# Kernel tuning notes

Measured on AMD Instinct MI355X. Metric: run time of the kernel, lower is better.

Reference implementation:

```python
import jax, jax.numpy as jnp
import numpy as np
import math

NUM_HEADS = 16
ROPE_BASE = 10000.0

def _rotate_half(t):
    d = t.shape[-1]
    x1, x2 = t[..., : d // 2], t[..., d // 2 :]
    return jnp.concatenate([-x2, x1], axis=-1)

def _rope_tables(seq_len, head_dim, dtype):
    inv_freq = 1.0 / (ROPE_BASE ** (jnp.arange(0, head_dim, 2, dtype=jnp.float32) / head_dim))
    t = jnp.arange(seq_len, dtype=jnp.float32)
    freqs = jnp.einsum('i,j->ij', t, inv_freq)          # [S, d/2]
    emb = jnp.concatenate([freqs, freqs], axis=-1)      # [S, d]
    return jnp.cos(emb).astype(dtype), jnp.sin(emb).astype(dtype)

def setup_inputs() -> dict:
    key = jax.random.key(0)
    ks = jax.random.split(key, 6)
    B, S, HID = 4, 2048, 1024
    x = jax.random.normal(ks[0], (B, S, HID), dtype=jnp.float32)
    w_scale = 0.02
    Wq = jax.random.normal(ks[1], (HID, HID), dtype=jnp.float32) * w_scale
    Wk = jax.random.normal(ks[2], (HID, HID), dtype=jnp.float32) * w_scale
    Wv = jax.random.normal(ks[3], (HID, HID), dtype=jnp.float32) * w_scale
    Wo = jax.random.normal(ks[4], (HID, HID), dtype=jnp.float32) * w_scale
    # ragged valid lengths in [S//2, S] so each sequence is non-trivial
    seq_lens = jax.random.randint(ks[5], (B,), S // 2, S + 1, dtype=jnp.int32)
    return {"x": x, "Wq": Wq, "Wk": Wk, "Wv": Wv, "Wo": Wo, "seq_lens": seq_lens}

def reference(x, Wq, Wk, Wv, Wo, seq_lens):
    B, S, HID = x.shape
    H = NUM_HEADS
    d = HID // H
    scale = 1.0 / math.sqrt(d)

    # qkv projections (nn.Linear, no bias)
    q = (x @ Wq).reshape(B, S, H, d)
    k = (x @ Wk).reshape(B, S, H, d)
    v = (x @ Wv).reshape(B, S, H, d)

    # fused RoPE, positions start at 0 for every sequence (prefill, beg=0)
    cos, sin = _rope_tables(S, d, x.dtype)              # [S, d]
    cos = cos[None, :, None, :]
    sin = sin[None, :, None, :]
    q = q * cos + _rotate_half(q) * sin
    k = k * cos + _rotate_half(k) * sin

    # causal SDPA over ragged batch via padding masks
    scores = jnp.einsum('bqhd,bkhd->bhqk', q, k) * scale  # [B,H,S,S]
    pos = jnp.arange(S)
    causal = pos[:, None] >= pos[None, :]                 # [S,S]
    valid_k = pos[None, :] < seq_lens[:, None]            # [B,S]
    mask = causal[None, None, :, :] & valid_k[:, None, None, :]
    neg = jnp.asarray(-1e9, dtype=scores.dtype)
    attn = jax.nn.softmax(jnp.where(mask, scores, neg), axis=-1)
    out = jnp.einsum('bhqk,bkhd->bqhd', attn, v).reshape(B, S, HID)

    out = out @ Wo
    # zero out padded query positions (they do not exist in CatTensor)
    valid_q = (pos[None, :] < seq_lens[:, None])[..., None]
    return jnp.where(valid_q, out, jnp.zeros((), dtype=out.dtype))
```

## Files before the change

kernel.cpp:

```cpp
#include <hip/hip_runtime.h>
#include <hip/hip_bf16.h>

typedef __attribute__((ext_vector_type(8))) short short8;
typedef __attribute__((ext_vector_type(4))) float f32x4;

constexpr int Bc   = 4;
constexpr int Sc   = 2048;
constexpr int HIDc = 1024;
constexpr int Hc   = 16;
constexpr size_t FB = (size_t)Bc * Sc * HIDc;
constexpr size_t WN = (size_t)HIDc * HIDc;

__device__ __forceinline__ int get_L(const int* seq, int b)
{
    return (seq[1] == 0) ? seq[2 * b] : seq[b];
}

__device__ __forceinline__ short f2bf(float v)
{
    __hip_bfloat16 h = __float2bfloat16(v);
    return *reinterpret_cast<short*>(&h);
}
__device__ __forceinline__ float bf2f(short s)
{
    __hip_bfloat16 h = *reinterpret_cast<__hip_bfloat16*>(&s);
    return __bfloat162float(h);
}
__device__ __forceinline__ unsigned pack2(short a, short b)
{
    return (unsigned)(unsigned short)a | ((unsigned)(unsigned short)b << 16);
}

__global__ __launch_bounds__(256) void split_pass(const float* __restrict__ in,
                                                  short* __restrict__ hi,
                                                  short* __restrict__ lo)
{
    const size_t i8 = ((size_t)blockIdx.x * 256 + threadIdx.x) * 8;
    const float4 u0 = *(const float4*)(in + i8);
    const float4 u1 = *(const float4*)(in + i8 + 4);
    const float v[8] = {u0.x, u0.y, u0.z, u0.w, u1.x, u1.y, u1.z, u1.w};
    short8 h, l;
#pragma unroll
    for (int j = 0; j < 8; j++) {
        const short hb = f2bf(v[j]);
        h[j] = hb;
        l[j] = f2bf(v[j] - bf2f(hb));
    }
    *(short8*)(hi + i8) = h;
    *(short8*)(lo + i8) = l;
}

__global__ __launch_bounds__(256) void rope_split(const float* __restrict__ p,
                                                  short* __restrict__ hi,
                                                  short* __restrict__ lo)
{
    const int idx = blockIdx.x * 256 + threadIdx.x;
    const int jc = idx & 3;
    const int h  = (idx >> 2) & 15;
    const int s  = (idx >> 6) & 2047;
    const int b  = idx >> 17;
    const int j0 = jc * 8;
    const size_t base = ((size_t)(b * Sc + s)) * HIDc + h * 64 + j0;

    const float4 a0 = *(const float4*)(p + base);
    const float4 a1 = *(const float4*)(p + base + 4);
    const float4 b0 = *(const float4*)(p + base + 32);
    const float4 b1 = *(const float4*)(p + base + 36);
    const float x1[8] = {a0.x, a0.y, a0.z, a0.w, a1.x, a1.y, a1.z, a1.w};
    const float x2[8] = {b0.x, b0.y, b0.z, b0.w, b1.x, b1.y, b1.z, b1.w};

    short8 h1, h2, l1, l2;
#pragma unroll
    for (int jj = 0; jj < 8; jj++) {
        const int j = j0 + jj;
        const float ang = (float)s * powf(10000.0f, -(float)j * (1.0f / 32.0f));
        const float cv = cosf(ang);
        const float sv = sinf(ang);
        const float y1 = x1[jj] * cv - x2[jj] * sv;
        const float y2 = x2[jj] * cv + x1[jj] * sv;
        const short hb1 = f2bf(y1), hb2 = f2bf(y2);
        h1[jj] = hb1; l1[jj] = f2bf(y1 - bf2f(hb1));
        h2[jj] = hb2; l2[jj] = f2bf(y2 - bf2f(hb2));
    }
    *(short8*)(hi + base)      = h1;
    *(short8*)(hi + base + 32) = h2;
    *(short8*)(lo + base)      = l1;
    *(short8*)(lo + base + 32) = l2;
}

__global__ __launch_bounds__(256) void vsplit_t(const float* __restrict__ V,
                                                short* __restrict__ th,
                                                short* __restrict__ tl)
{
    __shared__ float T[64][65];
    const int s0 = blockIdx.x * 64;
    const int h  = blockIdx.y & 15;
    const int b  = blockIdx.y >> 4;
    const int t  = threadIdx.x;
    const int r  = t >> 2;
    const int c  = (t & 3) * 16;
#pragma unroll
    for (int j = 0; j < 4; j++) {
        const float4 u = *(const float4*)(V + ((size_t)(b * Sc + s0 + r)) * HIDc + h * 64 + c + j * 4);
        T[r][c + j * 4 + 0] = u.x; T[r][c + j * 4 + 1] = u.y;
        T[r][c + j * 4 + 2] = u.z; T[r][c + j * 4 + 3] = u.w;
    }
    __syncthreads();
    short8 h0, h1, l0, l1;
#pragma unroll
    for (int j = 0; j < 8; j++) {
        const float v = T[c + j][r];
        const short hb = f2bf(v);
        h0[j] = hb; l0[j] = f2bf(v - bf2f(hb));
    }
#pragma unroll
    for (int j = 0; j < 8; j++) {
        const float v = T[c + 8 + j][r];
        const short hb = f2bf(v);
        h1[j] = hb; l1[j] = f2bf(v - bf2f(hb));
    }
    const size_t dst = ((size_t)(b * Hc + h) * 64 + r) * Sc + s0 + c;
    *(short8*)(th + dst)     = h0;
    *(short8*)(th + dst + 8) = h1;
    *(short8*)(tl + dst)     = l0;
    *(short8*)(tl + dst + 8) = l1;
}

__device__ __forceinline__ void wsplit_body(const float* __restrict__ W,
                                            short* __restrict__ th,
                                            short* __restrict__ tl,
                                            float (*T)[65])
{
    const int t  = threadIdx.x;
    const int n0 = blockIdx.x * 64;
    const int k0 = blockIdx.y * 64;
    const int r  = t >> 2;
    const int c  = (t & 3) * 16;
#pragma unroll
    for (int j = 0; j < 4; j++) {
        const float4 u = *(const float4*)(W + (size_t)(k0 + r) * HIDc + n0 + c + j * 4);
        T[r][c + j * 4 + 0] = u.x; T[r][c + j * 4 + 1] = u.y;
        T[r][c + j * 4 + 2] = u.z; T[r][c + j * 4 + 3] = u.w;
    }
    __syncthreads();
    short8 h0, h1, l0, l1;
#pragma unroll
    for (int j = 0; j < 8; j++) {
        const float v = T[c + j][r];
        const short hb = f2bf(v);
        h0[j] = hb; l0[j] = f2bf(v - bf2f(hb));
    }
#pragma unroll
    for (int j = 0; j < 8; j++) {
        const float v = T[c + 8 + j][r];
        const short hb = f2bf(v);
        h1[j] = hb; l1[j] = f2bf(v - bf2f(hb));
    }
    const size_t dst = (size_t)(n0 + r) * HIDc + k0 + c;
    *(short8*)(th + dst)     = h0;
    *(short8*)(th + dst + 8) = h1;
    *(short8*)(tl + dst)     = l0;
    *(short8*)(tl + dst + 8) = l1;
}

__global__ __launch_bounds__(256) void wsplit_t(const float* __restrict__ W,
                                                short* __restrict__ th,
                                                short* __restrict__ tl)
{
    __shared__ float T[64][65];
    wsplit_body(W, th, tl, T);
}

__global__ __launch_bounds__(256) void wsplit4_t(
    const float* __restrict__ W0, const float* __restrict__ W1,
    const float* __restrict__ W2, const float* __restrict__ W3,
    short* __restrict__ out)
{
    __shared__ float T[64][65];
    const int z = blockIdx.z;
    const float* W = (z == 0) ? W0 : (z == 1) ? W1 : (z == 2) ? W2 : W3;
    short* th = out + (size_t)z * 2 * WN;
    wsplit_body(W, th, th + WN, T);
}

__device__ __forceinline__ void gemm_x3_body(
    const short* __restrict__ Ah, const short* __restrict__ Al,
    const short* __restrict__ Bh, const short* __restrict__ Bl,
    float* __restrict__ C, const int* __restrict__ seq,
    const int m0, const int n0,
    short* AhS, short* AlS, short* BhS, short* BlS)
{
    const int t    = threadIdx.x;
    const int lane = t & 63;
    const int wid  = t >> 6;
    const int wr   = (wid >> 1) * 64;
    const int wc   = (wid & 1) * 64;
    const int lr   = lane & 15;
    const int lg   = lane >> 4;

    f32x4 acc[4][4];
#pragma unroll
    for (int mi = 0; mi < 4; mi++)
#pragma unroll
        for (int ni = 0; ni < 4; ni++) acc[mi][ni] = (f32x4)(0.f);

    for (int k0 = 0; k0 < HIDc; k0 += 64) {
        __syncthreads();
#pragma unroll
        for (int i = 0; i < 4; i++) {
            const int o  = i * 4096 + t * 16;
            const int r  = o >> 7;
            const int sc = (o & 127) ^ ((r & 7) << 4);
            const int k  = sc >> 1;
            const size_t ga = (size_t)(m0 + r) * HIDc + k0 + k;
            const size_t gb = (size_t)(n0 + r) * HIDc + k0 + k;
            __builtin_amdgcn_global_load_lds(
                (const __attribute__((address_space(1))) void*)(Ah + ga),
                (__attribute__((address_space(3))) void*)(AhS + (o >> 1)), 16, 0, 0);
            __builtin_amdgcn_global_load_lds(
                (const __attribute__((address_space(1))) void*)(Al + ga),
                (__attribute__((address_space(3))) void*)(AlS + (o >> 1)), 16, 0, 0);
            __builtin_amdgcn_global_load_lds(
                (const __attribute__((address_space(1))) void*)(Bh + gb),
                (__attribute__((address_space(3))) void*)(BhS + (o >> 1)), 16, 0, 0);
            __builtin_amdgcn_global_load_lds(
                (const __attribute__((address_space(1))) void*)(Bl + gb),
                (__attribute__((address_space(3))) void*)(BlS + (o >> 1)), 16, 0, 0);
        }
        __syncthreads();

        short8 a_h[4][2], a_l[4][2];
#pragma unroll
        for (int mi = 0; mi < 4; mi++) {
            const int r = wr + mi * 16 + lr;
#pragma unroll
            for (int kk = 0; kk < 2; kk++) {
                const int cb  = kk * 64 + lg * 16;
                const int off = r * 128 + (cb ^ ((r & 7) << 4));
                a_h[mi][kk] = *(const short8*)((const char*)AhS + off);
                a_l[mi][kk] = *(const short8*)((const char*)AlS + off);
            }
        }
#pragma unroll
        for (int ni = 0; ni < 4; ni++) {
            const int rn = wc + ni * 16 + lr;
            short8 b_h[2], b_l[2];
#pragma unroll
            for (int kk = 0; kk < 2; kk++) {
                const int cb  = kk * 64 + lg * 16;
                const int off = rn * 128 + (cb ^ ((rn & 7) << 4));
                b_h[kk] = *(const short8*)((const char*)BhS + off);
                b_l[kk] = *(const short8*)((const char*)BlS + off);
            }
#pragma unroll
            for (int mi = 0; mi < 4; mi++) {
#pragma unroll
                for (int kk = 0; kk < 2; kk++) {
                    acc[mi][ni] = __builtin_amdgcn_mfma_f32_16x16x32_bf16(
                        a_h[mi][kk], b_h[kk], acc[mi][ni], 0, 0, 0);
                    acc[mi][ni] = __builtin_amdgcn_mfma_f32_16x16x32_bf16(
                        a_h[mi][kk], b_l[kk], acc[mi][ni], 0, 0, 0);
                    acc[mi][ni] = __builtin_amdgcn_mfma_f32_16x16x32_bf16(
                        a_l[mi][kk], b_h[kk], acc[mi][ni], 0, 0, 0);
                }
            }
        }
    }

#pragma unroll
    for (int mi = 0; mi < 4; mi++) {
#pragma unroll
        for (int rr = 0; rr < 4; rr++) {
            const int row = m0 + wr + mi * 16 + lg * 4 + rr;
            bool zero = false;
            if (seq != nullptr) zero = ((row & 2047) >= get_L(seq, row >> 11));
#pragma unroll
            for (int ni = 0; ni < 4; ni++) {
                const float v = zero ? 0.f : acc[mi][ni][rr];
                C[(size_t)row * HIDc + n0 + wc + ni * 16 + lr] = v;
            }
        }
    }
}

__global__ __launch_bounds__(256, 2) void gemm_x3(
    const short* __restrict__ Ah, const short* __restrict__ Al,
    const short* __restrict__ Bh, const short* __restrict__ Bl,
    float* __restrict__ C, const int* __restrict__ seq)
{
    __shared__ alignas(16) short AhS[128 * 64];
    __shared__ alignas(16) short AlS[128 * 64];
    __shared__ alignas(16) short BhS[128 * 64];
    __shared__ alignas(16) short BlS[128 * 64];
    const int F   = blockIdx.x + 8 * blockIdx.y;
    const int xcd = F & 7;
    const int s   = F >> 3;
    const int ly  = xcd + 8 * (s >> 3);
    const int lx  = s & 7;
    gemm_x3_body(Ah, Al, Bh, Bl, C, seq, ly * 128, lx * 128,
                 AhS, AlS, BhS, BlS);
}

__global__ __launch_bounds__(256, 2) void gemm_x3_qkv(
    const short* __restrict__ Ah, const short* __restrict__ Al,
    const short* __restrict__ Wbase, float* __restrict__ Cbase)
{
    __shared__ alignas(16) short AhS[128 * 64];
    __shared__ alignas(16) short AlS[128 * 64];
    __shared__ alignas(16) short BhS[128 * 64];
    __shared__ alignas(16) short BlS[128 * 64];
    const int F   = blockIdx.x + 8 * blockIdx.y + 512 * blockIdx.z;
    const int xcd = F & 7;
    const int s   = F >> 3;
    const int ly  = xcd + 8 * (s / 24);
    const int rem = s % 24;
    const int lx  = rem & 7;
    const int lz  = rem >> 3;
    const short* Bh = Wbase + (size_t)lz * 2 * WN;
    gemm_x3_body(Ah, Al, Bh, Bh + WN, Cbase + (size_t)lz * FB,
                 nullptr, ly * 128, lx * 128, AhS, AlS, BhS, BlS);
}

__global__ __launch_bounds__(256, 3) void attn_mfma_sw(
    const short* __restrict__ Qh, const short* __restrict__ Ql,
    const short* __restrict__ Kh, const short* __restrict__ Kl,
    const short* __restrict__ Vth, const short* __restrict__ Vtl,
    short* __restrict__ Oh, short* __restrict__ Ol,
    const int* __restrict__ seq)
{
    __shared__ alignas(16) short KhS[64 * 64];
    __shared__ alignas(16) short KlS[64 * 64];
    __shared__ alignas(16) short VhS[64 * 64];
    __shared__ alignas(16) short VlS[64 * 64];
    __shared__ alignas(16) short PhS[4][16 * 64];
    __shared__ alignas(16) short PlS[4][16 * 64];

    const int blk  = blockIdx.x;
    const int bh   = blk & 63;
    const int qt   = 31 - (blk >> 6);
    const int h    = bh & 15;
    const int b    = bh >> 4;
    const int q0   = qt * 64;
    const int L    = get_L(seq, b);
    const int t    = threadIdx.x;
    const int w    = t >> 6;
    const int lane = t & 63;
    const int lr   = lane & 15;
    const int lg   = lane >> 4;

    if (q0 >= L) {
        const int r = t >> 2;
        const int c = (t & 3) * 16;
        const size_t base = ((size_t)(b * Sc + q0 + r)) * HIDc + h * 64 + c;
        const short8 z = {0, 0, 0, 0, 0, 0, 0, 0};
        *(short8*)(Oh + base)     = z;
        *(short8*)(Oh + base + 8) = z;
        *(short8*)(Ol + base)     = z;
        *(short8*)(Ol + base + 8) = z;
        return;
    }

    short8 qb_h[2], qb_l[2];
    {
        const size_t qrow = ((size_t)(b * Sc + q0 + w * 16 + lr)) * HIDc + h * 64;
        qb_h[0] = *(const short8*)(Qh + qrow + lg * 8);
        qb_h[1] = *(const short8*)(Qh + qrow + 32 + lg * 8);
        qb_l[0] = *(const short8*)(Ql + qrow + lg * 8);
        qb_l[1] = *(const short8*)(Ql + qrow + 32 + lg * 8);
    }

    f32x4 oacc[4];
#pragma unroll
    for (int t2 = 0; t2 < 4; t2++) oacc[t2] = (f32x4)(0.f);
    float m_s = -1.0e30f, l_s = 0.f;

    const int qpos = q0 + w * 16 + lr;

    const int kend = min(q0 + 64, L);
    for (int kb = 0; kb < kend; kb += 64) {
        __syncthreads();
#pragma unroll
        for (int i = 0; i < 2; i++) {
            const int o  = i * 4096 + t * 16;
            const int r  = o >> 7;
            const int sc = (o & 127) ^ ((r & 7) << 4);
            const int k  = sc >> 1;
            const size_t gk = ((size_t)(b * Sc + kb + r)) * HIDc + h * 64 + k;
            const size_t gv = ((size_t)(b * Hc + h) * 64 + r) * Sc + kb + k;
            __builtin_amdgcn_global_load_lds(
                (const __attribute__((address_space(1))) void*)(Kh + gk),
                (__attribute__((address_space(3))) void*)((char*)KhS + o), 16, 0, 0);
            __builtin_amdgcn_global_load_lds(
                (const __attribute__((address_space(1))) void*)(Kl + gk),
                (__attribute__((address_space(3))) void*)((char*)KlS + o), 16, 0, 0);
            __builtin_amdgcn_global_load_lds(
                (const __attribute__((address_space(1))) void*)(Vth + gv),
                (__attribute__((address_space(3))) void*)((char*)VhS + o), 16, 0, 0);
            __builtin_amdgcn_global_load_lds(
                (const __attribute__((address_space(1))) void*)(Vtl + gv),
                (__attribute__((address_space(3))) void*)((char*)VlS + o), 16, 0, 0);
        }
        __syncthreads();

        f32x4 s4[4];
#pragma unroll
        for (int tt = 0; tt < 4; tt++) s4[tt] = (f32x4)(0.f);
        __builtin_amdgcn_s_setprio(1);
#pragma unroll
        for (int tt = 0; tt < 4; tt++) {
            const int rn = tt * 16 + lr;
#pragma unroll
            for (int kk = 0; kk < 2; kk++) {
                const int off = rn * 128 + ((kk * 64 + lg * 16) ^ ((rn & 7) << 4));
                const short8 ka_h = *(const short8*)((const char*)KhS + off);
                const short8 ka_l = *(const short8*)((const char*)KlS + off);
                s4[tt] = __builtin_amdgcn_mfma_f32_16x16x32_bf16(ka_h, qb_h[kk], s4[tt], 0, 0, 0);
                s4[tt] = __builtin_amdgcn_mfma_f32_16x16x32_bf16(ka_h, qb_l[kk], s4[tt], 0, 0, 0);
                s4[tt] = __builtin_amdgcn_mfma_f32_16x16x32_bf16(ka_l, qb_h[kk], s4[tt], 0, 0, 0);
            }
        }
        __builtin_amdgcn_s_setprio(0);

        float tmax = -1.0e30f;
#pragma unroll
        for (int tt = 0; tt < 4; tt++)
#pragma unroll
            for (int r = 0; r < 4; r++) {
                const int kpos = kb + tt * 16 + lg * 4 + r;
                const bool valid = (kpos <= qpos) && (kpos < L);
                const float v = valid ? s4[tt][r] * 0.125f : -1.0e9f;
                s4[tt][r] = v;
                tmax = fmaxf(tmax, v);
            }
        tmax = fmaxf(tmax, __shfl_xor(tmax, 16));
        tmax = fmaxf(tmax, __shfl_xor(tmax, 32));
        const float mnew  = fmaxf(m_s, tmax);
        const float alpha = __expf(m_s - mnew);
        float psum = 0.f;
#pragma unroll
        for (int tt = 0; tt < 4; tt++)
#pragma unroll
            for (int r = 0; r < 4; r++) {
                const float e = __expf(s4[tt][r] - mnew);
                s4[tt][r] = e;
                psum += e;
            }
        psum += __shfl_xor(psum, 16);
        psum += __shfl_xor(psum, 32);
        l_s = alpha * l_s + psum;
        m_s = mnew;

#pragma unroll
        for (int r = 0; r < 4; r++) {
            const float ar = __shfl(alpha, lg * 4 + r);
#pragma unroll
            for (int t2 = 0; t2 < 4; t2++) oacc[t2][r] *= ar;
        }

#pragma unroll
        for (int tt = 0; tt < 4; tt++) {
            const short h0 = f2bf(s4[tt][0]); const short l0 = f2bf(s4[tt][0] - bf2f(h0));
            const short h1 = f2bf(s4[tt][1]); const short l1 = f2bf(s4[tt][1] - bf2f(h1));
            const short h2 = f2bf(s4[tt][2]); const short l2 = f2bf(s4[tt][2] - bf2f(h2));
            const short h3 = f2bf(s4[tt][3]); const short l3 = f2bf(s4[tt][3] - bf2f(h3));
            const int off = lr * 128 + ((tt * 32 + lg * 8) ^ ((lr & 7) << 4));
            uint2 uh; uh.x = pack2(h0, h1); uh.y = pack2(h2, h3);
            uint2 ul; ul.x = pack2(l0, l1); ul.y = pack2(l2, l3);
            *(uint2*)((char*)&PhS[w][0] + off) = uh;
            *(uint2*)((char*)&PlS[w][0] + off) = ul;
        }

        __builtin_amdgcn_sched_barrier(0);

        short8 pa_h[2], pa_l[2];
#pragma unroll
        for (int kk = 0; kk < 2; kk++) {
            const int poff = lr * 128 + ((kk * 64 + lg * 16) ^ ((lr & 7) << 4));
            pa_h[kk] = *(const short8*)((const char*)&PhS[w][0] + poff);
            pa_l[kk] = *(const short8*)((const char*)&PlS[w][0] + poff);
        }
        __builtin_amdgcn_s_setprio(1);
#pragma unroll
        for (int t2 = 0; t2 < 4; t2++) {
            const int rv = t2 * 16 + lr;
#pragma unroll
            for (int kk = 0; kk < 2; kk++) {
                const int voff = rv * 128 + ((kk * 64 + lg * 16) ^ ((rv & 7) << 4));
                const short8 vb_h = *(const short8*)((const char*)VhS + voff);
                const short8 vb_l = *(const short8*)((const char*)VlS + voff);
                oacc[t2] = __builtin_amdgcn_mfma_f32_16x16x32_bf16(pa_h[kk], vb_h, oacc[t2], 0, 0, 0);
                oacc[t2] = __builtin_amdgcn_mfma_f32_16x16x32_bf16(pa_h[kk], vb_l, oacc[t2], 0, 0, 0);
                oacc[t2] = __builtin_amdgcn_mfma_f32_16x16x32_bf16(pa_l[kk], vb_h, oacc[t2], 0, 0, 0);
            }
        }
        __builtin_amdgcn_s_setprio(0);
    }

#pragma unroll
    for (int r = 0; r < 4; r++) {
        const float lrow = __shfl(l_s, lg * 4 + r);
        const float inv  = 1.0f / lrow;
        const int   row  = q0 + w * 16 + lg * 4 + r;
        const size_t base = ((size_t)(b * Sc + row)) * HIDc + h * 64;
#pragma unroll
        for (int t2 = 0; t2 < 4; t2++) {
            const float v = oacc[t2][r] * inv;
            const short hb = f2bf(v);
            Oh[base + t2 * 16 + lr] = hb;
            Ol[base + t2 * 16 + lr] = f2bf(v - bf2f(hb));
        }
    }
}

__global__ __launch_bounds__(256) void gemm64(
    const float* __restrict__ A, const float* __restrict__ W,
    float* __restrict__ C, const int K, const int N,
    const int* __restrict__ seq)
{
    __shared__ float As[32][68];
    __shared__ float Bs[32][68];

    const int t  = threadIdx.x;
    const int m0 = blockIdx.y * 64;
    const int n0 = blockIdx.x * 64;
    const int ty = t >> 4, tx = t & 15;
    const int ar = t >> 2;
    const int ac = (t & 3) * 8;
    const int wr = t >> 3;
    const int wc = (t & 7) * 8;

    float acc[4][4];
#pragma unroll
    for (int i = 0; i < 4; i++)
#pragma unroll
        for (int j = 0; j < 4; j++) acc[i][j] = 0.f;

    for (int k0 = 0; k0 < K; k0 += 32) {
        __syncthreads();
        {
            const float* p = A + (size_t)(m0 + ar) * K + k0 + ac;
            const float4 u0 = *(const float4*)p;
            const float4 u1 = *(const float4*)(p + 4);
            As[ac + 0][ar] = u0.x; As[ac + 1][ar] = u0.y;
            As[ac + 2][ar] = u0.z; As[ac + 3][ar] = u0.w;
            As[ac + 4][ar] = u1.x; As[ac + 5][ar] = u1.y;
            As[ac + 6][ar] = u1.z; As[ac + 7][ar] = u1.w;
        }
        {
            const float* p = W + (size_t)(k0 + wr) * N + n0 + wc;
            const float4 u0 = *(const float4*)p;
            const float4 u1 = *(const float4*)(p + 4);
            *(float4*)&Bs[wr][wc]     = u0;
            *(float4*)&Bs[wr][wc + 4] = u1;
        }
        __syncthreads();

#pragma unroll 8
        for (int kk = 0; kk < 32; kk++) {
            const float4 a4 = *(const float4*)&As[kk][ty * 4];
            const float4 b4 = *(const float4*)&Bs[kk][tx * 4];
            const float av[4] = {a4.x, a4.y, a4.z, a4.w};
            const float bv[4] = {b4.x, b4.y, b4.z, b4.w};
#pragma unroll
            for (int i = 0; i < 4; i++)
#pragma unroll
                for (int j = 0; j < 4; j++)
                    acc[i][j] = fmaf(av[i], bv[j], acc[i][j]);
        }
    }

#pragma unroll
    for (int i = 0; i < 4; i++) {
        const int row = m0 + ty * 4 + i;
        bool zero = false;
        if (seq != nullptr) zero = ((row & 2047) >= get_L(seq, row >> 11));
#pragma unroll
        for (int j = 0; j < 4; j++) {
            const float v = zero ? 0.f : acc[i][j];
            C[(size_t)row * N + n0 + tx * 4 + j] = v;
        }
    }
}

__global__ __launch_bounds__(256) void rope_pair(float* __restrict__ p)
{
    const int idx = blockIdx.x * 256 + threadIdx.x;
    const int j = idx & 31;
    const int h = (idx >> 5) & 15;
    const int s = (idx >> 9) & 2047;
    const int b = idx >> 20;
    const size_t base = ((size_t)(b * Sc + s)) * HIDc + h * 64 + j;

    const float x1 = p[base];
    const float x2 = p[base + 32];
    const float ang = (float)s * powf(10000.0f, -(float)j * (1.0f / 32.0f));
    const float cv = cosf(ang);
    const float sv = sinf(ang);
    p[base]      = x1 * cv - x2 * sv;
    p[base + 32] = x2 * cv + x1 * sv;
}

__device__ __forceinline__ int swz(int r, int chunk)
{
    return (((chunk ^ (r >> 2)) & 15) << 2);
}

__global__ __launch_bounds__(256) void attn64(
    const float* Q, const float* __restrict__ K,
    const float* __restrict__ V, float* O,
    const int* __restrict__ seq)
{
    __shared__ float Qs[64][64];
    __shared__ float Ks[64][64];
    __shared__ float Vs[64][64];

    const int blk = blockIdx.x;
    const int bh  = blk & 63;
    const int qt  = 31 - (blk >> 6);
    const int h   = bh & 15;
    const int b   = bh >> 4;
    const int q0  = qt * 64;
    const int L   = get_L(seq, b);
    const int t   = threadIdx.x;
    const int qg  = t >> 4;
    const int kg  = t & 15;

    if (q0 >= L) {
#pragma unroll
        for (int i = 0; i < 4; i++) {
            const size_t row = (size_t)(b * Sc + q0 + qg * 4 + i);
#pragma unroll
            for (int c = 0; c < 4; c++)
                O[row * HIDc + h * 64 + kg * 4 + c] = 0.f;
        }
        return;
    }

    {
        const int r = t >> 2;
        const int c = (t & 3) * 16;
        const float* src = Q + ((size_t)(b * Sc + q0 + r)) * HIDc + h * 64 + c;
#pragma unroll
        for (int jj = 0; jj < 4; jj++)
            *(float4*)&Qs[r][swz(r, (c >> 2) + jj)] = *(const float4*)(src + 4 * jj);
    }

    float m_i[4], l_i[4], acc[4][4];
#pragma unroll
    for (int i = 0; i < 4; i++) {
        m_i[i] = -1.0e30f; l_i[i] = 0.f;
#pragma unroll
        for (int c = 0; c < 4; c++) acc[i][c] = 0.f;
    }

    const int kend = min(q0 + 64, L);
    for (int kb = 0; kb < kend; kb += 64) {
        __syncthreads();
        {
            const int r = t >> 2;
            const int c = (t & 3) * 16;
            const size_t off = ((size_t)(b * Sc + kb + r)) * HIDc + h * 64 + c;
#pragma unroll
            for (int jj = 0; jj < 4; jj++)
                *(float4*)&Ks[r][swz(r, (c >> 2) + jj)] = *(const float4*)(K + off + 4 * jj);
#pragma unroll
            for (int jj = 0; jj < 4; jj++)
                *(float4*)&Vs[r][swz(r, (c >> 2) + jj)] = *(const float4*)(V + off + 4 * jj);
        }
        __syncthreads();

        float s[4][4];
#pragma unroll
        for (int i = 0; i < 4; i++)
#pragma unroll
            for (int c = 0; c < 4; c++) s[i][c] = 0.f;

#pragma unroll 4
        for (int dc = 0; dc < 64; dc += 4) {
            float4 q4[4], k4[4];
#pragma unroll
            for (int i = 0; i < 4; i++)
                q4[i] = *(const float4*)&Qs[qg * 4 + i][swz(qg * 4 + i, dc >> 2)];
#pragma unroll
            for (int c = 0; c < 4; c++)
                k4[c] = *(const float4*)&Ks[kg * 4 + c][swz(kg * 4 + c, dc >> 2)];
#pragma unroll
            for (int i = 0; i < 4; i++)
#pragma unroll
                for (int c = 0; c < 4; c++) {
                    s[i][c] = fmaf(q4[i].x, k4[c].x, s[i][c]);
                    s[i][c] = fmaf(q4[i].y, k4[c].y, s[i][c]);
                    s[i][c] = fmaf(q4[i].z, k4[c].z, s[i][c]);
                    s[i][c] = fmaf(q4[i].w, k4[c].w, s[i][c]);
                }
        }

#pragma unroll
        for (int i = 0; i < 4; i++) {
            const int qpos = q0 + qg * 4 + i;
#pragma unroll
            for (int c = 0; c < 4; c++) {
                const int kpos = kb + kg * 4 + c;
                const bool valid = (kpos <= qpos) && (kpos < L);
                s[i][c] = valid ? s[i][c] * 0.125f : -1.0e9f;
            }
        }

#pragma unroll
        for (int i = 0; i < 4; i++) {
            float tm = fmaxf(fmaxf(s[i][0], s[i][1]), fmaxf(s[i][2], s[i][3]));
#pragma unroll
            for (int off = 1; off < 16; off <<= 1)
                tm = fmaxf(tm, __shfl_xor(tm, off));
            const float mnew  = fmaxf(m_i[i], tm);
            const float alpha = __expf(m_i[i] - mnew);

            float psum = 0.f;
#pragma unroll
            for (int c = 0; c < 4; c++) {
                s[i][c] = __expf(s[i][c] - mnew);
                psum += s[i][c];
            }
#pragma unroll
            for (int off = 1; off < 16; off <<= 1)
                psum += __shfl_xor(psum, off);

            l_i[i] = alpha * l_i[i] + psum;
            m_i[i] = mnew;
#pragma unroll
            for (int c = 0; c < 4; c++) acc[i][c] *= alpha;
        }

        __syncthreads();
#pragma unroll
        for (int i = 0; i < 4; i++)
#pragma unroll
            for (int c = 0; c < 4; c++) {
                const int pr = kg * 4 + c;
                Ks[pr][swz(pr, qg) + i] = s[i][c];
            }
        __syncthreads();

#pragma unroll 4
        for (int ki = 0; ki < 64; ki++) {
            const float4 p4 = *(const float4*)&Ks[ki][swz(ki, qg)];
            const float4 v4 = *(const float4*)&Vs[ki][swz(ki, kg)];
            const float pv[4] = {p4.x, p4.y, p4.z, p4.w};
            const float vv[4] = {v4.x, v4.y, v4.z, v4.w};
#pragma unroll
            for (int i = 0; i < 4; i++)
#pragma unroll
                for (int c = 0; c < 4; c++)
                    acc[i][c] = fmaf(pv[i], vv[c], acc[i][c]);
        }
    }

#pragma unroll
    for (int i = 0; i < 4; i++) {
        const float inv = 1.0f / l_i[i];
        const size_t row = (size_t)(b * Sc + q0 + qg * 4 + i);
#pragma unroll
        for (int c = 0; c < 4; c++)
            O[row * HIDc + h * 64 + kg * 4 + c] = acc[i][c] * inv;
    }
}

extern "C" void kernel_launch(void* const* d_in, const int* in_sizes, int n_in,
                              void* d_out, int out_size, void* d_ws, size_t ws_size,
                              hipStream_t stream)
{
    const float* x   = (const float*)d_in[0];
    const float* Wq  = (const float*)d_in[1];
    const float* Wk  = (const float*)d_in[2];
    const float* Wv  = (const float*)d_in[3];
    const float* Wo  = (const float*)d_in[4];
    const int*   seq = (const int*)d_in[5];

    const size_t needX3 = 3 * FB * sizeof(float) + 2 * WN * sizeof(short);
    const size_t needX4 = 3 * FB * sizeof(float) + 8 * WN * sizeof(short);

    const dim3 gg(HIDc / 128, Bc * Sc / 128);
    const int  sb  = (int)(FB / (8 * 256));
    const int  rsb = (int)(FB / (16 * 256));

    if (ws_size >= needX4) {
        float* Qf = (float*)d_ws;
        float* Kf = Qf + FB;
        float* Vf = Kf + FB;
        short* ws_s = (short*)d_ws;
        short* W4 = ws_s + 6 * FB;

        short* xh = (short*)d_out;
        short* xl = xh + FB;

        split_pass<<<sb, 256, 0, stream>>>(x, xh, xl);
        wsplit4_t<<<dim3(16, 16, 4), 256, 0, stream>>>(Wq, Wk, Wv, Wo, W4);
        gemm_x3_qkv<<<dim3(8, 64, 3), 256, 0, stream>>>(xh, xl, W4, Qf);

        short* Qh2 = (short*)d_out;
        short* Ql2 = Qh2 + FB;
        rope_split<<<rsb, 256, 0, stream>>>(Qf, Qh2, Ql2);
        short* Kh2 = ws_s;
        short* Kl2 = Kh2 + FB;
        rope_split<<<rsb, 256, 0, stream>>>(Kf, Kh2, Kl2);
        short* Vth = ws_s + 2 * FB;
        short* Vtl = Vth + FB;
        vsplit_t<<<dim3(32, 64), 256, 0, stream>>>(Vf, Vth, Vtl);

        short* Oh2 = ws_s + 4 * FB;
        short* Ol2 = Oh2 + FB;
        attn_mfma_sw<<<Bc * Hc * (Sc / 64), 256, 0, stream>>>(
            Qh2, Ql2, Kh2, Kl2, Vth, Vtl, Oh2, Ol2, seq);

        gemm_x3<<<gg, 256, 0, stream>>>(Oh2, Ol2, W4 + 6 * WN, W4 + 7 * WN,
                                        (float*)d_out, seq);
    } else if (ws_size >= needX3) {
        float* Qf = (float*)d_ws;
        float* Kf = Qf + FB;
        float* Vf = Kf + FB;
        short* ws_s = (short*)d_ws;
        short* wh = ws_s + 6 * FB;
        short* wl = wh + WN;

        short* xh = (short*)d_out;
        short* xl = xh + FB;

        const dim3 wg(16, 16);

        split_pass<<<sb, 256, 0, stream>>>(x, xh, xl);

        wsplit_t<<<wg, 256, 0, stream>>>(Wq, wh, wl);
        gemm_x3<<<gg, 256, 0, stream>>>(xh, xl, wh, wl, Qf, nullptr);
        wsplit_t<<<wg, 256, 0, stream>>>(Wk, wh, wl);
        gemm_x3<<<gg, 256, 0, stream>>>(xh, xl, wh, wl, Kf, nullptr);
        wsplit_t<<<wg, 256, 0, stream>>>(Wv, wh, wl);
        gemm_x3<<<gg, 256, 0, stream>>>(xh, xl, wh, wl, Vf, nullptr);

        short* Qh2 = (short*)d_out;
        short* Ql2 = Qh2 + FB;
        rope_split<<<rsb, 256, 0, stream>>>(Qf, Qh2, Ql2);
        short* Kh2 = ws_s;
        short* Kl2 = Kh2 + FB;
        rope_split<<<rsb, 256, 0, stream>>>(Kf, Kh2, Kl2);
        short* Vth = ws_s + 2 * FB;
        short* Vtl = Vth + FB;
        vsplit_t<<<dim3(32, 64), 256, 0, stream>>>(Vf, Vth, Vtl);

        short* Oh2 = ws_s + 4 * FB;
        short* Ol2 = Oh2 + FB;
        attn_mfma_sw<<<Bc * Hc * (Sc / 64), 256, 0, stream>>>(
            Qh2, Ql2, Kh2, Kl2, Vth, Vtl, Oh2, Ol2, seq);

        wsplit_t<<<wg, 256, 0, stream>>>(Wo, wh, wl);
        gemm_x3<<<gg, 256, 0, stream>>>(Oh2, Ol2, wh, wl, (float*)d_out, seq);
    } else if (ws_size >= 3 * FB * sizeof(float)) {
        float* Q = (float*)d_ws;
        float* K = Q + FB;
        float* V = K + FB;

        const dim3 g64(HIDc / 64, Bc * Sc / 64);
        gemm64<<<g64, 256, 0, stream>>>(x, Wq, Q, HIDc, HIDc, nullptr);
        gemm64<<<g64, 256, 0, stream>>>(x, Wk, K, HIDc, HIDc, nullptr);
        gemm64<<<g64, 256, 0, stream>>>(x, Wv, V, HIDc, HIDc, nullptr);

        const int rb = Bc * Sc * Hc * 32 / 256;
        rope_pair<<<rb, 256, 0, stream>>>(Q);
        rope_pair<<<rb, 256, 0, stream>>>(K);

        attn64<<<Bc * Hc * (Sc / 64), 256, 0, stream>>>(Q, K, V, Q, seq);

        gemm64<<<g64, 256, 0, stream>>>(Q, Wo, (float*)d_out, HIDc, HIDc, seq);
    } else {
        hipMemsetAsync(d_out, 0, (size_t)out_size * sizeof(float), stream);
    }
}
```

Measured before the change: 420.3 us.

## Enlarge attention query tile to 128 rows, two 16-row groups per wave

The attention kernel now handles 128 query rows per block instead of 64. Each wave processes two 16-row query groups, so every K/V tile loaded into shared memory is reused across twice as many queries, which halves K/V global traffic and block count. The cost is roughly double the register use per thread (launch bounds drop from 3 to 2 waves per SIMD), larger P staging in LDS, and coarser causal tiles that add some masked work on the diagonal.

```diff
diff --git a/kernel.cpp b/kernel.cpp
--- a/kernel.cpp
+++ b/kernel.cpp
@@ -321,7 +321,7 @@
                  nullptr, ly * 128, lx * 128, AhS, AlS, BhS, BlS);
 }
 
-__global__ __launch_bounds__(256, 3) void attn_mfma_sw(
+__global__ __launch_bounds__(256, 2) void attn_sw128(
     const short* __restrict__ Qh, const short* __restrict__ Ql,
     const short* __restrict__ Kh, const short* __restrict__ Kl,
     const short* __restrict__ Vth, const short* __restrict__ Vtl,
@@ -332,15 +332,15 @@
     __shared__ alignas(16) short KlS[64 * 64];
     __shared__ alignas(16) short VhS[64 * 64];
     __shared__ alignas(16) short VlS[64 * 64];
-    __shared__ alignas(16) short PhS[4][16 * 64];
-    __shared__ alignas(16) short PlS[4][16 * 64];
+    __shared__ alignas(16) short PhS[4][2][16 * 64];
+    __shared__ alignas(16) short PlS[4][2][16 * 64];
 
     const int blk  = blockIdx.x;
     const int bh   = blk & 63;
-    const int qt   = 31 - (blk >> 6);
+    const int qt   = 15 - (blk >> 6);
     const int h    = bh & 15;
     const int b    = bh >> 4;
-    const int q0   = qt * 64;
+    const int q0   = qt * 128;
     const int L    = get_L(seq, b);
     const int t    = threadIdx.x;
     const int w    = t >> 6;
@@ -349,34 +349,38 @@
     const int lg   = lane >> 4;
 
     if (q0 >= L) {
-        const int r = t >> 2;
-        const int c = (t & 3) * 16;
+        const int r = t >> 1;
+        const int c = (t & 1) * 32;
         const size_t base = ((size_t)(b * Sc + q0 + r)) * HIDc + h * 64 + c;
         const short8 z = {0, 0, 0, 0, 0, 0, 0, 0};
-        *(short8*)(Oh + base)     = z;
-        *(short8*)(Oh + base + 8) = z;
-        *(short8*)(Ol + base)     = z;
-        *(short8*)(Ol + base + 8) = z;
+#pragma unroll
+        for (int j = 0; j < 4; j++) {
+            *(short8*)(Oh + base + 8 * j) = z;
+            *(short8*)(Ol + base + 8 * j) = z;
+        }
         return;
     }
 
-    short8 qb_h[2], qb_l[2];
-    {
-        const size_t qrow = ((size_t)(b * Sc + q0 + w * 16 + lr)) * HIDc + h * 64;
-        qb_h[0] = *(const short8*)(Qh + qrow + lg * 8);
-        qb_h[1] = *(const short8*)(Qh + qrow + 32 + lg * 8);
-        qb_l[0] = *(const short8*)(Ql + qrow + lg * 8);
-        qb_l[1] = *(const short8*)(Ql + qrow + 32 + lg * 8);
-    }
-
-    f32x4 oacc[4];
-#pragma unroll
-    for (int t2 = 0; t2 < 4; t2++) oacc[t2] = (f32x4)(0.f);
-    float m_s = -1.0e30f, l_s = 0.f;
-
-    const int qpos = q0 + w * 16 + lr;
-
-    const int kend = min(q0 + 64, L);
+    short8 qb_h[2][2], qb_l[2][2];
+#pragma unroll
+    for (int g = 0; g < 2; g++) {
+        const size_t qrow = ((size_t)(b * Sc + q0 + w * 32 + g * 16 + lr)) * HIDc + h * 64;
+        qb_h[g][0] = *(const short8*)(Qh + qrow + lg * 8);
+        qb_h[g][1] = *(const short8*)(Qh + qrow + 32 + lg * 8);
+        qb_l[g][0] = *(const short8*)(Ql + qrow + lg * 8);
+        qb_l[g][1] = *(const short8*)(Ql + qrow + 32 + lg * 8);
+    }
+
+    f32x4 oacc[2][4];
+    float m_s[2], l_s[2];
+#pragma unroll
+    for (int g = 0; g < 2; g++) {
+        m_s[g] = -1.0e30f; l_s[g] = 0.f;
+#pragma unroll
+        for (int t2 = 0; t2 < 4; t2++) oacc[g][t2] = (f32x4)(0.f);
+    }
+
+    const int kend = min(q0 + 128, L);
     for (int kb = 0; kb < kend; kb += 64) {
         __syncthreads();
 #pragma unroll
@@ -402,9 +406,11 @@
         }
         __syncthreads();
 
-        f32x4 s4[4];
-#pragma unroll
-        for (int tt = 0; tt < 4; tt++) s4[tt] = (f32x4)(0.f);
+        f32x4 s4[2][4];
+#pragma unroll
+        for (int g = 0; g < 2; g++)
+#pragma unroll
+            for (int tt = 0; tt < 4; tt++) s4[g][tt] = (f32x4)(0.f);
         __builtin_amdgcn_s_setprio(1);
 #pragma unroll
         for (int tt = 0; tt < 4; tt++) {
@@ -414,71 +420,81 @@
                 const int off = rn * 128 + ((kk * 64 + lg * 16) ^ ((rn & 7) << 4));
                 const short8 ka_h = *(const short8*)((const char*)KhS + off);
                 const short8 ka_l = *(const short8*)((const char*)KlS + off);
-                s4[tt] = __builtin_amdgcn_mfma_f32_16x16x32_bf16(ka_h, qb_h[kk], s4[tt], 0, 0, 0);
-                s4[tt] = __builtin_amdgcn_mfma_f32_16x16x32_bf16(ka_h, qb_l[kk], s4[tt], 0, 0, 0);
-                s4[tt] = __builtin_amdgcn_mfma_f32_16x16x32_bf16(ka_l, qb_h[kk], s4[tt], 0, 0, 0);
+#pragma unroll
+                for (int g = 0; g < 2; g++) {
+                    s4[g][tt] = __builtin_amdgcn_mfma_f32_16x16x32_bf16(ka_h, qb_h[g][kk], s4[g][tt], 0, 0, 0);
+                    s4[g][tt] = __builtin_amdgcn_mfma_f32_16x16x32_bf16(ka_h, qb_l[g][kk], s4[g][tt], 0, 0, 0);
+                    s4[g][tt] = __builtin_amdgcn_mfma_f32_16x16x32_bf16(ka_l, qb_h[g][kk], s4[g][tt], 0, 0, 0);
+                }
             }
         }
         __builtin_amdgcn_s_setprio(0);
 
-        float tmax = -1.0e30f;
-#pragma unroll
-        for (int tt = 0; tt < 4; tt++)
+#pragma unroll
+        for (int g = 0; g < 2; g++) {
+            const int qpos = q0 + w * 32 + g * 16 + lr;
+            float tmax = -1.0e30f;
+#pragma unroll
+            for (int tt = 0; tt < 4; tt++)
+#pragma unroll
+                for (int r = 0; r < 4; r++) {
+                    const int kpos = kb + tt * 16 + lg * 4 + r;
+                    const bool valid = (kpos <= qpos) && (kpos < L);
+                    const float v = valid ? s4[g][tt][r] * 0.125f : -1.0e9f;
+                    s4[g][tt][r] = v;
+                    tmax = fmaxf(tmax, v);
+                }
+            tmax = fmaxf(tmax, __shfl_xor(tmax, 16));
+            tmax = fmaxf(tmax, __shfl_xor(tmax, 32));
+            const float mnew  = fmaxf(m_s[g], tmax);
+            const float alpha = __expf(m_s[g] - mnew);
+            float psum = 0.f;
+#pragma unroll
+            for (int tt = 0; tt < 4; tt++)
+#pragma unroll
+                for (int r = 0; r < 4; r++) {
+                    const float e = __expf(s4[g][tt][r] - mnew);
+                    s4[g][tt][r] = e;
+                    psum += e;
+                }
+            psum += __shfl_xor(psum, 16);
+            psum += __shfl_xor(psum, 32);
+            l_s[g] = alpha * l_s[g] + psum;
+            m_s[g] = mnew;
+
 #pragma unroll
             for (int r = 0; r < 4; r++) {
-                const int kpos = kb + tt * 16 + lg * 4 + r;
-                const bool valid = (kpos <= qpos) && (kpos < L);
-                const float v = valid ? s4[tt][r] * 0.125f : -1.0e9f;
-                s4[tt][r] = v;
-                tmax = fmaxf(tmax, v);
-            }
-        tmax = fmaxf(tmax, __shfl_xor(tmax, 16));
-        tmax = fmaxf(tmax, __shfl_xor(tmax, 32));
-        const float mnew  = fmaxf(m_s, tmax);
-        const float alpha = __expf(m_s - mnew);
-        float psum = 0.f;
-#pragma unroll
-        for (int tt = 0; tt < 4; tt++)
-#pragma unroll
-            for (int r = 0; r < 4; r++) {
-                const float e = __expf(s4[tt][r] - mnew);
-                s4[tt][r] = e;
-                psum += e;
-            }
-        psum += __shfl_xor(psum, 16);
-        psum += __shfl_xor(psum, 32);
-        l_s = alpha * l_s + psum;
-        m_s = mnew;
-
-#pragma unroll
-        for (int r = 0; r < 4; r++) {
-            const float ar = __shfl(alpha, lg * 4 + r);
-#pragma unroll
-            for (int t2 = 0; t2 < 4; t2++) oacc[t2][r] *= ar;
-        }
-
-#pragma unroll
-        for (int tt = 0; tt < 4; tt++) {
-            const short h0 = f2bf(s4[tt][0]); const short l0 = f2bf(s4[tt][0] - bf2f(h0));
-            const short h1 = f2bf(s4[tt][1]); const short l1 = f2bf(s4[tt][1] - bf2f(h1));
-            const short h2 = f2bf(s4[tt][2]); const short l2 = f2bf(s4[tt][2] - bf2f(h2));
-            const short h3 = f2bf(s4[tt][3]); const short l3 = f2bf(s4[tt][3] - bf2f(h3));
-            const int off = lr * 128 + ((tt * 32 + lg * 8) ^ ((lr & 7) << 4));
-            uint2 uh; uh.x = pack2(h0, h1); uh.y = pack2(h2, h3);
-            uint2 ul; ul.x = pack2(l0, l1); ul.y = pack2(l2, l3);
-            *(uint2*)((char*)&PhS[w][0] + off) = uh;
-            *(uint2*)((char*)&PlS[w][0] + off) = ul;
+                const float ar = __shfl(alpha, lg * 4 + r);
+#pragma unroll
+                for (int t2 = 0; t2 < 4; t2++) oacc[g][t2][r] *= ar;
+            }
+
+#pragma unroll
+            for (int tt = 0; tt < 4; tt++) {
+                const short h0 = f2bf(s4[g][tt][0]); const short l0 = f2bf(s4[g][tt][0] - bf2f(h0));
+                const short h1 = f2bf(s4[g][tt][1]); const short l1 = f2bf(s4[g][tt][1] - bf2f(h1));
+                const short h2 = f2bf(s4[g][tt][2]); const short l2 = f2bf(s4[g][tt][2] - bf2f(h2));
+                const short h3 = f2bf(s4[g][tt][3]); const short l3 = f2bf(s4[g][tt][3] - bf2f(h3));
+                const int off = lr * 128 + ((tt * 32 + lg * 8) ^ ((lr & 7) << 4));
+                uint2 uh; uh.x = pack2(h0, h1); uh.y = pack2(h2, h3);
+                uint2 ul; ul.x = pack2(l0, l1); ul.y = pack2(l2, l3);
+                *(uint2*)((char*)&PhS[w][g][0] + off) = uh;
+                *(uint2*)((char*)&PlS[w][g][0] + off) = ul;
+            }
         }
 
         __builtin_amdgcn_sched_barrier(0);
 
-        short8 pa_h[2], pa_l[2];
-#pragma unroll
-        for (int kk = 0; kk < 2; kk++) {
-            const int poff = lr * 128 + ((kk * 64 + lg * 16) ^ ((lr & 7) << 4));
-            pa_h[kk] = *(const short8*)((const char*)&PhS[w][0] + poff);
-            pa_l[kk] = *(const short8*)((const char*)&PlS[w][0] + poff);
-        }
+        short8 pa_h[2][2], pa_l[2][2];
+#pragma unroll
+        for (int g = 0; g < 2; g++)
+#pragma unroll
+            for (int kk = 0; kk < 2; kk++) {
+                const int poff = lr * 128 + ((kk * 64 + lg * 16) ^ ((lr & 7) << 4));
+                pa_h[g][kk] = *(const short8*)((const char*)&PhS[w][g][0] + poff);
+                pa_l[g][kk] = *(const short8*)((const char*)&PlS[w][g][0] + poff);
+            }
+
         __builtin_amdgcn_s_setprio(1);
 #pragma unroll
         for (int t2 = 0; t2 < 4; t2++) {
@@ -488,28 +504,33 @@
                 const int voff = rv * 128 + ((kk * 64 + lg * 16) ^ ((rv & 7) << 4));
                 const short8 vb_h = *(const short8*)((const char*)VhS + voff);
                 const short8 vb_l = *(const short8*)((const char*)VlS + voff);
-                oacc[t2] = __builtin_amdgcn_mfma_f32_16x16x32_bf16(pa_h[kk], vb_h, oacc[t2], 0, 0, 0);
-                oacc[t2] = __builtin_amdgcn_mfma_f32_16x16x32_bf16(pa_h[kk], vb_l, oacc[t2], 0, 0, 0);
-                oacc[t2] = __builtin_amdgcn_mfma_f32_16x16x32_bf16(pa_l[kk], vb_h, oacc[t2], 0, 0, 0);
+#pragma unroll
+                for (int g = 0; g < 2; g++) {
+                    oacc[g][t2] = __builtin_amdgcn_mfma_f32_16x16x32_bf16(pa_h[g][kk], vb_h, oacc[g][t2], 0, 0, 0);
+                    oacc[g][t2] = __builtin_amdgcn_mfma_f32_16x16x32_bf16(pa_h[g][kk], vb_l, oacc[g][t2], 0, 0, 0);
+                    oacc[g][t2] = __builtin_amdgcn_mfma_f32_16x16x32_bf16(pa_l[g][kk], vb_h, oacc[g][t2], 0, 0, 0);
+                }
             }
         }
         __builtin_amdgcn_s_setprio(0);
     }
 
 #pragma unroll
-    for (int r = 0; r < 4; r++) {
-        const float lrow = __shfl(l_s, lg * 4 + r);
-        const float inv  = 1.0f / lrow;
-        const int   row  = q0 + w * 16 + lg * 4 + r;
-        const size_t base = ((size_t)(b * Sc + row)) * HIDc + h * 64;
-#pragma unroll
-        for (int t2 = 0; t2 < 4; t2++) {
-            const float v = oacc[t2][r] * inv;
-            const short hb = f2bf(v);
-            Oh[base + t2 * 16 + lr] = hb;
-            Ol[base + t2 * 16 + lr] = f2bf(v - bf2f(hb));
-        }
-    }
+    for (int g = 0; g < 2; g++)
+#pragma unroll
+        for (int r = 0; r < 4; r++) {
+            const float lrow = __shfl(l_s[g], lg * 4 + r);
+            const float inv  = 1.0f / lrow;
+            const int   row  = q0 + w * 32 + g * 16 + lg * 4 + r;
+            const size_t base = ((size_t)(b * Sc + row)) * HIDc + h * 64;
+#pragma unroll
+            for (int t2 = 0; t2 < 4; t2++) {
+                const float v = oacc[g][t2][r] * inv;
+                const short hb = f2bf(v);
+                Oh[base + t2 * 16 + lr] = hb;
+                Ol[base + t2 * 16 + lr] = f2bf(v - bf2f(hb));
+            }
+        }
 }
 
 __global__ __launch_bounds__(256) void gemm64(
@@ -809,7 +830,7 @@
 
         short* Oh2 = ws_s + 4 * FB;
         short* Ol2 = Oh2 + FB;
-        attn_mfma_sw<<<Bc * Hc * (Sc / 64), 256, 0, stream>>>(
+        attn_sw128<<<Bc * Hc * (Sc / 128), 256, 0, stream>>>(
             Qh2, Ql2, Kh2, Kl2, Vth, Vtl, Oh2, Ol2, seq);
 
         gemm_x3<<<gg, 256, 0, stream>>>(Oh2, Ol2, W4 + 6 * WN, W4 + 7 * WN,
@@ -848,7 +869,7 @@
 
         short* Oh2 = ws_s + 4 * FB;
         short* Ol2 = Oh2 + FB;
-        attn_mfma_sw<<<Bc * Hc * (Sc / 64), 256, 0, stream>>>(
+        attn_sw128<<<Bc * Hc * (Sc / 128), 256, 0, stream>>>(
             Qh2, Ql2, Kh2, Kl2, Vth, Vtl, Oh2, Ol2, seq);
 
         wsplit_t<<<wg, 256, 0, stream>>>(Wo, wh, wl);
```

Result: no change. 425.2 us (+1.2%).

## Fuse RoPE and bf16 hi/lo split into QKV GEMM epilogue

Applied to the files above, without the earlier changes.

Adds a precomputed cos/sin table kernel and rewrites the QKV GEMM epilogue so Q and K get RoPE applied and are written directly as bf16 hi/lo pairs. V is still written in fp32 for the transpose-split. This removes the two separate rope_split passes and the fp32 Q/K round trip through global memory. In exchange the epilogue does 2-byte strided stores and extra table loads, and the workspace layout and buffer aliasing are rearranged.

```diff
diff --git a/kernel.cpp b/kernel.cpp
--- a/kernel.cpp
+++ b/kernel.cpp
@@ -10,6 +10,7 @@
 constexpr int Hc   = 16;
 constexpr size_t FB = (size_t)Bc * Sc * HIDc;
 constexpr size_t WN = (size_t)HIDc * HIDc;
+constexpr size_t TB = (size_t)Sc * 32;
 
 __device__ __forceinline__ int get_L(const int* seq, int b)
 {
@@ -29,6 +30,17 @@
 __device__ __forceinline__ unsigned pack2(short a, short b)
 {
     return (unsigned)(unsigned short)a | ((unsigned)(unsigned short)b << 16);
+}
+
+__global__ __launch_bounds__(256) void rope_tab(float* __restrict__ ct,
+                                                float* __restrict__ st)
+{
+    const int idx = blockIdx.x * 256 + threadIdx.x;
+    const int s = idx >> 5;
+    const int j = idx & 31;
+    const float ang = (float)s * powf(10000.0f, -(float)j * (1.0f / 32.0f));
+    ct[idx] = cosf(ang);
+    st[idx] = sinf(ang);
 }
 
 __global__ __launch_bounds__(256) void split_pass(const float* __restrict__ in,
@@ -183,12 +195,12 @@
     wsplit_body(W, th, th + WN, T);
 }
 
-__device__ __forceinline__ void gemm_x3_body(
+__device__ __forceinline__ void gemm_x3_acc(
     const short* __restrict__ Ah, const short* __restrict__ Al,
     const short* __restrict__ Bh, const short* __restrict__ Bl,
-    float* __restrict__ C, const int* __restrict__ seq,
     const int m0, const int n0,
-    short* AhS, short* AlS, short* BhS, short* BlS)
+    short* AhS, short* AlS, short* BhS, short* BlS,
+    f32x4 (&acc)[4][4])
 {
     const int t    = threadIdx.x;
     const int lane = t & 63;
@@ -198,7 +210,6 @@
     const int lr   = lane & 15;
     const int lg   = lane >> 4;
 
-    f32x4 acc[4][4];
 #pragma unroll
     for (int mi = 0; mi < 4; mi++)
 #pragma unroll
@@ -266,21 +277,6 @@
             }
         }
     }
-
-#pragma unroll
-    for (int mi = 0; mi < 4; mi++) {
-#pragma unroll
-        for (int rr = 0; rr < 4; rr++) {
-            const int row = m0 + wr + mi * 16 + lg * 4 + rr;
-            bool zero = false;
-            if (seq != nullptr) zero = ((row & 2047) >= get_L(seq, row >> 11));
-#pragma unroll
-            for (int ni = 0; ni < 4; ni++) {
-                const float v = zero ? 0.f : acc[mi][ni][rr];
-                C[(size_t)row * HIDc + n0 + wc + ni * 16 + lr] = v;
-            }
-        }
-    }
 }
 
 __global__ __launch_bounds__(256, 2) void gemm_x3(
@@ -297,13 +293,38 @@
     const int s   = F >> 3;
     const int ly  = xcd + 8 * (s >> 3);
     const int lx  = s & 7;
-    gemm_x3_body(Ah, Al, Bh, Bl, C, seq, ly * 128, lx * 128,
-                 AhS, AlS, BhS, BlS);
-}
-
-__global__ __launch_bounds__(256, 2) void gemm_x3_qkv(
+    const int m0 = ly * 128, n0 = lx * 128;
+
+    f32x4 acc[4][4];
+    gemm_x3_acc(Ah, Al, Bh, Bl, m0, n0, AhS, AlS, BhS, BlS, acc);
+
+    const int lane = threadIdx.x & 63;
+    const int wid  = threadIdx.x >> 6;
+    const int wr   = (wid >> 1) * 64;
+    const int wc   = (wid & 1) * 64;
+    const int lr   = lane & 15;
+    const int lg   = lane >> 4;
+#pragma unroll
+    for (int mi = 0; mi < 4; mi++) {
+#pragma unroll
+        for (int rr = 0; rr < 4; rr++) {
+            const int row = m0 + wr + mi * 16 + lg * 4 + rr;
+            bool zero = false;
+            if (seq != nullptr) zero = ((row & 2047) >= get_L(seq, row >> 11));
+#pragma unroll
+            for (int ni = 0; ni < 4; ni++) {
+                const float v = zero ? 0.f : acc[mi][ni][rr];
+                C[(size_t)row * HIDc + n0 + wc + ni * 16 + lr] = v;
+            }
+        }
+    }
+}
+
+__global__ __launch_bounds__(256, 2) void gemm_x3_qkv_rope(
     const short* __restrict__ Ah, const short* __restrict__ Al,
-    const short* __restrict__ Wbase, float* __restrict__ Cbase)
+    const short* __restrict__ Wbase, short* __restrict__ outS,
+    float* __restrict__ outF,
+    const float* __restrict__ cos_t, const float* __restrict__ sin_t)
 {
     __shared__ alignas(16) short AhS[128 * 64];
     __shared__ alignas(16) short AlS[128 * 64];
@@ -316,9 +337,61 @@
     const int rem = s % 24;
     const int lx  = rem & 7;
     const int lz  = rem >> 3;
+    const int m0 = ly * 128, n0 = lx * 128;
     const short* Bh = Wbase + (size_t)lz * 2 * WN;
-    gemm_x3_body(Ah, Al, Bh, Bh + WN, Cbase + (size_t)lz * FB,
-                 nullptr, ly * 128, lx * 128, AhS, AlS, BhS, BlS);
+
+    f32x4 acc[4][4];
+    gemm_x3_acc(Ah, Al, Bh, Bh + WN, m0, n0, AhS, AlS, BhS, BlS, acc);
+
+    const int lane = threadIdx.x & 63;
+    const int wid  = threadIdx.x >> 6;
+    const int wr   = (wid >> 1) * 64;
+    const int wc   = (wid & 1) * 64;
+    const int lr   = lane & 15;
+    const int lg   = lane >> 4;
+
+    if (lz < 2) {
+        short* Ch = outS + (size_t)lz * 2 * FB;
+        short* Cl = Ch + FB;
+#pragma unroll
+        for (int mi = 0; mi < 4; mi++) {
+#pragma unroll
+            for (int rr = 0; rr < 4; rr++) {
+                const int row = m0 + wr + mi * 16 + lg * 4 + rr;
+                const int sp  = row & 2047;
+                const float c0  = cos_t[sp * 32 + lr];
+                const float sn0 = sin_t[sp * 32 + lr];
+                const float c1  = cos_t[sp * 32 + 16 + lr];
+                const float sn1 = sin_t[sp * 32 + 16 + lr];
+                const float x0 = acc[mi][0][rr];
+                const float x1 = acc[mi][1][rr];
+                const float x2 = acc[mi][2][rr];
+                const float x3 = acc[mi][3][rr];
+                const float y[4] = {x0 * c0 - x2 * sn0,
+                                    x1 * c1 - x3 * sn1,
+                                    x2 * c0 + x0 * sn0,
+                                    x3 * c1 + x1 * sn1};
+                const size_t cb = (size_t)row * HIDc + n0 + wc + lr;
+#pragma unroll
+                for (int ni = 0; ni < 4; ni++) {
+                    const short hb = f2bf(y[ni]);
+                    Ch[cb + ni * 16] = hb;
+                    Cl[cb + ni * 16] = f2bf(y[ni] - bf2f(hb));
+                }
+            }
+        }
+    } else {
+#pragma unroll
+        for (int mi = 0; mi < 4; mi++) {
+#pragma unroll
+            for (int rr = 0; rr < 4; rr++) {
+                const int row = m0 + wr + mi * 16 + lg * 4 + rr;
+#pragma unroll
+                for (int ni = 0; ni < 4; ni++)
+                    outF[(size_t)row * HIDc + n0 + wc + ni * 16 + lr] = acc[mi][ni][rr];
+            }
+        }
+    }
 }
 
 __global__ __launch_bounds__(256, 3) void attn_mfma_sw(
@@ -778,12 +851,45 @@
 
     const size_t needX3 = 3 * FB * sizeof(float) + 2 * WN * sizeof(short);
     const size_t needX4 = 3 * FB * sizeof(float) + 8 * WN * sizeof(short);
+    const size_t needX5 = needX4 + 2 * TB * sizeof(float);
 
     const dim3 gg(HIDc / 128, Bc * Sc / 128);
     const int  sb  = (int)(FB / (8 * 256));
     const int  rsb = (int)(FB / (16 * 256));
 
-    if (ws_size >= needX4) {
+    if (ws_size >= needX5) {
+        short* ws_s = (short*)d_ws;
+        short* W4   = ws_s + 6 * FB;
+        float* cosT = (float*)(ws_s + 6 * FB + 8 * WN);
+        float* sinT = cosT + TB;
+
+        short* xh = (short*)d_out;
+        short* xl = xh + FB;
+
+        rope_tab<<<(int)(TB / 256), 256, 0, stream>>>(cosT, sinT);
+        split_pass<<<sb, 256, 0, stream>>>(x, xh, xl);
+        wsplit4_t<<<dim3(16, 16, 4), 256, 0, stream>>>(Wq, Wk, Wv, Wo, W4);
+
+        float* Vf = (float*)(ws_s + 4 * FB);
+        gemm_x3_qkv_rope<<<dim3(8, 64, 3), 256, 0, stream>>>(
+            xh, xl, W4, ws_s, Vf, cosT, sinT);
+
+        short* Vth = (short*)d_out;
+        short* Vtl = Vth + FB;
+        vsplit_t<<<dim3(32, 64), 256, 0, stream>>>(Vf, Vth, Vtl);
+
+        short* Qh2 = ws_s;
+        short* Ql2 = Qh2 + FB;
+        short* Kh2 = ws_s + 2 * FB;
+        short* Kl2 = Kh2 + FB;
+        short* Oh2 = ws_s + 4 * FB;
+        short* Ol2 = Oh2 + FB;
+        attn_mfma_sw<<<Bc * Hc * (Sc / 64), 256, 0, stream>>>(
+            Qh2, Ql2, Kh2, Kl2, Vth, Vtl, Oh2, Ol2, seq);
+
+        gemm_x3<<<gg, 256, 0, stream>>>(Oh2, Ol2, W4 + 6 * WN, W4 + 7 * WN,
+                                        (float*)d_out, seq);
+    } else if (ws_size >= needX4) {
         float* Qf = (float*)d_ws;
         float* Kf = Qf + FB;
         float* Vf = Kf + FB;
@@ -795,7 +901,11 @@
 
         split_pass<<<sb, 256, 0, stream>>>(x, xh, xl);
         wsplit4_t<<<dim3(16, 16, 4), 256, 0, stream>>>(Wq, Wk, Wv, Wo, W4);
-        gemm_x3_qkv<<<dim3(8, 64, 3), 256, 0, stream>>>(xh, xl, W4, Qf);
+        {
+            gemm_x3<<<gg, 256, 0, stream>>>(xh, xl, W4 + 0 * WN, W4 + 1 * WN, Qf, nullptr);
+            gemm_x3<<<gg, 256, 0, stream>>>(xh, xl, W4 + 2 * WN, W4 + 3 * WN, Kf, nullptr);
+            gemm_x3<<<gg, 256, 0, stream>>>(xh, xl, W4 + 4 * WN, W4 + 5 * WN, Vf, nullptr);
+        }
 
         short* Qh2 = (short*)d_out;
         short* Ql2 = Qh2 + FB;
```

New measurement: 379.4 us. 9.7% less time.
